# Kernel tuning notes

Hardware: AMD Instinct MI355X
Metric: run time of the kernel (lower is better)

The kernel has to match this reference:

```python
import jax, jax.numpy as jnp
import numpy as np

N_USER = 50000
N_ITEM = 50000
E = 500000
D_IN = 256
H = 4
D_HID = 64
D_OUT = 128
NEG_SLOPE = 0.2  # DGL GATConv default leaky_relu slope


def setup_inputs() -> dict:
    key = jax.random.key(0)
    ks = jax.random.split(key, 14)
    f = lambda k, s: jax.random.normal(k, s, dtype=jnp.float32)
    return {
        "h_src_user": f(ks[0], (N_USER, D_IN)),
        "h_src_item": f(ks[1], (N_ITEM, D_IN)),
        "h_dst_user": f(ks[2], (N_USER, D_IN)),
        "h_dst_item": f(ks[3], (N_ITEM, D_IN)),
        "u2i_src": jax.random.randint(ks[4], (E,), 0, N_USER),
        "u2i_dst": jax.random.randint(ks[5], (E,), 0, N_ITEM),
        "i2u_src": jax.random.randint(ks[6], (E,), 0, N_ITEM),
        "i2u_dst": jax.random.randint(ks[7], (E,), 0, N_USER),
        "fc_w": f(ks[8], (D_IN, H * D_HID)) * 0.05,
        "attn_l": f(ks[9], (H, D_HID)) * 0.05,
        "attn_r": f(ks[10], (H, D_HID)) * 0.05,
        "gat_bias": jnp.zeros((H * D_HID,), jnp.float32),
        "W_w": f(ks[11], (D_IN + D_HID, D_OUT)) * 0.05,
        "W_b": jnp.zeros((D_OUT,), jnp.float32),
    }


def _gat(feat_src, feat_dst, src, dst, n_dst, fc_w, attn_l, attn_r, gat_bias):
    # DGL GATConv (dropout is identity in eval mode)
    H_, D_ = attn_l.shape
    fs = (feat_src @ fc_w).reshape(-1, H_, D_)  # [Ns,H,D]
    fd = (feat_dst @ fc_w).reshape(-1, H_, D_)  # [Nd,H,D]
    el = jnp.sum(fs * attn_l, axis=-1)          # [Ns,H]
    er = jnp.sum(fd * attn_r, axis=-1)          # [Nd,H]
    e = jax.nn.leaky_relu(el[src] + er[dst], NEG_SLOPE)  # [E,H]
    # edge softmax per (dst node, head)
    m = jax.ops.segment_max(e, dst, num_segments=n_dst)
    m = jnp.where(jnp.isfinite(m), m, 0.0)      # guard zero-degree dst
    ex = jnp.exp(e - m[dst])
    den = jax.ops.segment_sum(ex, dst, num_segments=n_dst)
    alpha = ex / jnp.where(den == 0, 1.0, den)[dst]      # [E,H]
    out = jax.ops.segment_sum(alpha[:, :, None] * fs[src], dst, num_segments=n_dst)
    return out + gat_bias.reshape(1, H_, D_)    # [Nd,H,D]


def _head(agg, h_dst, W_w, W_b):
    # mean over heads, concat with dst feats, linear+relu, safe L2 normalize
    z = jax.nn.relu(jnp.concatenate([agg.mean(axis=1), h_dst], axis=1) @ W_w + W_b)
    n = jnp.linalg.norm(z, axis=1, keepdims=True)
    return z / jnp.where(n == 0, 1.0, n)


def reference(h_src_user, h_src_item, h_dst_user, h_dst_item,
              u2i_src, u2i_dst, i2u_src, i2u_dst,
              fc_w, attn_l, attn_r, gat_bias, W_w, W_b):
    agg_item = _gat(h_src_user, h_dst_item, u2i_src, u2i_dst, N_ITEM, fc_w, attn_l, attn_r, gat_bias)
    agg_user = _gat(h_src_item, h_dst_user, i2u_src, i2u_dst, N_USER, fc_w, attn_l, attn_r, gat_bias)
    z_user = _head(agg_user, h_dst_user, W_w, W_b)
    z_item = _head(agg_item, h_dst_item, W_w, W_b)
    return z_user, z_item
```

## Files before the change

### kernel.cpp

```cpp
#include <hip/hip_runtime.h>

#define NN 50000
#define N2 100000
#define EE 500000
#define E2 1000000

typedef unsigned short u16;
typedef unsigned int u32;

typedef __attribute__((ext_vector_type(8))) __bf16 bf16x8;
typedef __attribute__((ext_vector_type(4))) float f32x4;

__device__ __forceinline__ float4 ld4(const float* p) { return *(const float4*)p; }

__device__ __forceinline__ u16 f2bf(float f) {
  u32 u = __float_as_uint(f);
  u += 0x7FFFu + ((u >> 16) & 1u);
  return (u16)(u >> 16);
}

__device__ __forceinline__ u32 cvtpk(float lo, float hi) {
  u32 r;
  asm("v_cvt_pk_bf16_f32 %0, %1, %2" : "=v"(r) : "v"(lo), "v"(hi));
  return r;
}

__global__ void L384_const(const float* fc_w, const float* attn_l,
                           const float* attn_r, const float* Ww, float* w_r,
                           u16* wlB, u16* Bt, u16* Wt) {
  const int b = blockIdx.x;
  const int t = threadIdx.x;
  if (b < 256) {
    Bt[b * 256 + t] = f2bf(fc_w[(size_t)t * 256 + b]);
  } else if (b == 256) {
    for (int h = 0; h < 4; ++h) {
      float sl = 0.f, sr = 0.f;
      for (int d = 0; d < 64; ++d) {
        float f = fc_w[t * 256 + h * 64 + d];
        sl += f * attn_l[h * 64 + d];
        sr += f * attn_r[h * 64 + d];
      }
      w_r[t * 4 + h] = sr;
      wlB[h * 256 + t] = f2bf(sl);
    }
    for (int h = 4; h < 16; ++h) wlB[h * 256 + t] = 0;
  } else {
    int n = b - 257;
    for (int k = t; k < 320; k += 256)
      Wt[(size_t)n * 320 + k] = f2bf(Ww[(size_t)k * 128 + n]);
  }
}

__global__ void L384_prep(const float* Du, const float* Di, const float* w_r_,
                          u16* X, float* er) {
  const int r = blockIdx.x * 4 + (threadIdx.x >> 6);
  const int lane = threadIdx.x & 63;
  if (r >= N2) return;
  const float* src = (r < NN) ? Du + (size_t)r * 256 : Di + (size_t)(r - NN) * 256;
  float4 xv = ld4(src + lane * 4);
  uint2 pk = make_uint2(cvtpk(xv.x, xv.y), cvtpk(xv.z, xv.w));
  *(uint2*)(X + (size_t)r * 320 + 64 + lane * 4) = pk;
  const float* wr = w_r_ + lane * 16;
  float4 w0 = ld4(wr), w1 = ld4(wr + 4), w2 = ld4(wr + 8), w3 = ld4(wr + 12);
  float a0 = xv.x * w0.x + xv.y * w1.x + xv.z * w2.x + xv.w * w3.x;
  float a1 = xv.x * w0.y + xv.y * w1.y + xv.z * w2.y + xv.w * w3.y;
  float a2 = xv.x * w0.z + xv.y * w1.z + xv.z * w2.z + xv.w * w3.z;
  float a3 = xv.x * w0.w + xv.y * w1.w + xv.z * w2.w + xv.w * w3.w;
  for (int off = 32; off; off >>= 1) {
    a0 += __shfl_xor(a0, off);
    a1 += __shfl_xor(a1, off);
    a2 += __shfl_xor(a2, off);
    a3 += __shfl_xor(a3, off);
  }
  if (lane == 0) {
    float* op = er + (size_t)r * 4;
    op[0] = a0; op[1] = a1; op[2] = a2; op[3] = a3;
  }
}

__global__ __launch_bounds__(512) void L384_gemm(const float* Au, const float* Ai,
                                                 const u16* Bt, const u16* wlB,
                                                 u16* C, float* el) {
  __shared__ u16 bs[64][264];
  const int t = threadIdx.x;
  const int w = t >> 6;
  const int l = t & 63;
  const int lr = l & 15;
  const int kg = l >> 4;
  const int row0 = blockIdx.x * 128;

  const int row = row0 + w * 16 + lr;
  const int rr = (row < N2) ? row : (N2 - 1);
  const float* arow =
      ((rr < NN) ? Au + (size_t)rr * 256 : Ai + (size_t)(rr - NN) * 256) + kg * 8;
  uint4 a[8];
#pragma unroll
  for (int ks = 0; ks < 8; ++ks) {
    float4 f0 = ld4(arow + ks * 32);
    float4 f1 = ld4(arow + ks * 32 + 4);
    a[ks] = make_uint4(cvtpk(f0.x, f0.y), cvtpk(f0.z, f0.w), cvtpk(f1.x, f1.y),
                       cvtpk(f1.z, f1.w));
  }

  {
    f32x4 eacc = {0.f, 0.f, 0.f, 0.f};
    const u16* wl = wlB + lr * 256 + kg * 8;
#pragma unroll
    for (int ks = 0; ks < 8; ++ks) {
      union { bf16x8 v; uint4 q; } af, wf;
      af.q = a[ks];
      wf.q = *(const uint4*)(wl + ks * 32);
      eacc = __builtin_amdgcn_mfma_f32_16x16x32_bf16(af.v, wf.v, eacc, 0, 0, 0);
    }
    if (lr < 4) {
#pragma unroll
      for (int r = 0; r < 4; ++r) {
        int grow = row0 + w * 16 + kg * 4 + r;
        if (grow < N2) el[(size_t)grow * 4 + lr] = eacc[r];
      }
    }
  }

  for (int strip = 0; strip < 4; ++strip) {
    __syncthreads();
    {
      const int brow = t >> 3;
      const int bc = (t & 7) * 32;
      const uint4* s = (const uint4*)(Bt + (size_t)(strip * 64 + brow) * 256 + bc);
      uint4* d = (uint4*)&bs[brow][bc];
      d[0] = s[0]; d[1] = s[1]; d[2] = s[2]; d[3] = s[3];
    }
    __syncthreads();

    f32x4 acc[4];
#pragma unroll
    for (int ct = 0; ct < 4; ++ct) acc[ct] = (f32x4){0.f, 0.f, 0.f, 0.f};
#pragma unroll
    for (int ks = 0; ks < 8; ++ks) {
      union { bf16x8 v; uint4 q; } af;
      af.q = a[ks];
#pragma unroll
      for (int ct = 0; ct < 4; ++ct) {
        union { bf16x8 v; uint4 q; } b;
        b.q = *(const uint4*)&bs[ct * 16 + lr][ks * 32 + kg * 8];
        acc[ct] = __builtin_amdgcn_mfma_f32_16x16x32_bf16(af.v, b.v, acc[ct], 0, 0, 0);
      }
    }

#pragma unroll
    for (int p = 0; p < 2; ++p) {
      __syncthreads();
      if ((w >> 2) == p) {
        const int lrow = (w & 3) * 16 + kg * 4;
#pragma unroll
        for (int ct = 0; ct < 4; ++ct)
#pragma unroll
          for (int r = 0; r < 4; ++r)
            bs[lrow + r][ct * 16 + lr] = f2bf(acc[ct][r]);
      }
      __syncthreads();
      const int lrow2 = t >> 3;
      const int c0 = (t & 7) * 8;
      const int grow = row0 + p * 64 + lrow2;
      if (grow < N2)
        *(uint4*)(C + (size_t)grow * 256 + strip * 64 + c0) =
            *(const uint4*)&bs[lrow2][c0];
    }
  }
}

__global__ void L384_zero(int* p, int n) {
  int i = blockIdx.x * 256 + threadIdx.x;
  if (i < n) p[i] = 0;
}
__global__ void L384_hist(const int* i2u_dst, const int* u2i_dst, int* cnt) {
  int e = blockIdx.x * 256 + threadIdx.x;
  if (e < EE) {
    int d = i2u_dst[e];
    d = ((unsigned)d < NN) ? d : 0;
    atomicAdd(&cnt[d], 1);
  } else if (e < E2) {
    int d = u2i_dst[e - EE];
    d = ((unsigned)d < NN) ? d : 0;
    atomicAdd(&cnt[NN + d], 1);
  }
}
__global__ void L384_scan1(const int* cnt, int* part, int* bsum, int n) {
  __shared__ int sh[256];
  const int t = threadIdx.x;
  const int base = blockIdx.x * 1024 + t * 4;
  int v0 = (base + 0 < n) ? cnt[base + 0] : 0;
  int v1 = (base + 1 < n) ? cnt[base + 1] : 0;
  int v2 = (base + 2 < n) ? cnt[base + 2] : 0;
  int v3 = (base + 3 < n) ? cnt[base + 3] : 0;
  int s0 = v0, s1 = s0 + v1, s2 = s1 + v2, s3 = s2 + v3;
  sh[t] = s3;
  __syncthreads();
  for (int off = 1; off < 256; off <<= 1) {
    int x = (t >= off) ? sh[t - off] : 0;
    __syncthreads();
    sh[t] += x;
    __syncthreads();
  }
  int excl = (t > 0) ? sh[t - 1] : 0;
  if (base + 0 < n) part[base + 0] = excl;
  if (base + 1 < n) part[base + 1] = excl + s0;
  if (base + 2 < n) part[base + 2] = excl + s1;
  if (base + 3 < n) part[base + 3] = excl + s2;
  if (t == 255) bsum[blockIdx.x] = sh[255];
}
__global__ void L384_scan2(int* bsum, int nb, int* indptr, int n) {
  if (threadIdx.x == 0 && blockIdx.x == 0) {
    int acc = 0;
    for (int i = 0; i < nb; ++i) {
      int c = bsum[i];
      bsum[i] = acc;
      acc += c;
    }
    indptr[n] = acc;
  }
}
__global__ void L384_scan3(int* indptr, const int* bsum, int* cur, int n) {
  int i = blockIdx.x * 256 + threadIdx.x;
  if (i < n) {
    int v = indptr[i] + bsum[i >> 10];
    indptr[i] = v;
    cur[i] = v;
  }
}
__global__ void L384_fill(const int* i2u_src, const int* i2u_dst,
                          const int* u2i_src, const int* u2i_dst,
                          int* cur, int* csr) {
  int e = blockIdx.x * 256 + threadIdx.x;
  if (e < EE) {
    int d = i2u_dst[e];
    d = ((unsigned)d < NN) ? d : 0;
    int s = i2u_src[e];
    s = ((unsigned)s < NN) ? s : 0;
    int pos = atomicAdd(&cur[d], 1);
    if ((unsigned)pos < E2) csr[pos] = NN + s;
  } else if (e < E2) {
    int d = u2i_dst[e - EE];
    d = ((unsigned)d < NN) ? d : 0;
    int s = u2i_src[e - EE];
    s = ((unsigned)s < NN) ? s : 0;
    int pos = atomicAdd(&cur[NN + d], 1);
    if ((unsigned)pos < E2) csr[pos] = s;
  }
}
__global__ void L384_sort(const int* indptr, int* csr, int n) {
  __shared__ int buf[5120];
  const int t = threadIdx.x;
  const int node0 = blockIdx.x * 256;
  const int nEnd = (node0 + 256 < n) ? (node0 + 256) : n;
  if (node0 >= n) return;
  const int segL = indptr[node0];
  const int segR = indptr[nEnd];
  const int len = segR - segL;
  if (len <= 5120) {
    for (int i = t; i < len; i += 256) buf[i] = csr[segL + i];
    __syncthreads();
    const int node = node0 + t;
    if (node < n) {
      int p0 = indptr[node] - segL;
      int p1 = indptr[node + 1] - segL;
      for (int a = p0 + 1; a < p1; ++a) {
        int v = buf[a];
        int b = a - 1;
        while (b >= p0 && buf[b] > v) {
          buf[b + 1] = buf[b];
          --b;
        }
        buf[b + 1] = v;
      }
    }
    __syncthreads();
    for (int i = t; i < len; i += 256) csr[segL + i] = buf[i];
  } else {
    const int node = node0 + t;
    if (node < n) {
      int p0 = indptr[node], p1 = indptr[node + 1];
      for (int a = p0 + 1; a < p1; ++a) {
        int v = csr[a];
        int b = a - 1;
        while (b >= p0 && csr[b] > v) {
          csr[b + 1] = csr[b];
          --b;
        }
        csr[b + 1] = v;
      }
    }
  }
}

__global__ void L384_aggx(const int* indptr, const int* csr, const float* el,
                          const float* er, const u16* fs, const float* bias,
                          float* alphaG, u16* X) {
  __shared__ float aL[4][64][4];
  __shared__ int sL[4][64];
  const int slot = threadIdx.x >> 6;
  const int wid = blockIdx.x * 4 + slot;
  const int lane = threadIdx.x & 63;
  if (wid >= N2) return;
  const int p0 = indptr[wid];
  const int deg = indptr[wid + 1] - p0;
  const int h = lane >> 4;
  const int c = lane & 15;
  float4 er4 = ld4(er + (size_t)wid * 4);

  const bool small = (deg <= 64);
  if (small) {
    float4 ex = {0.f, 0.f, 0.f, 0.f};
    int s = 0;
    if (lane < deg) {
      s = csr[p0 + lane];
      s = ((unsigned)s < N2) ? s : 0;
      float4 ev = ld4(el + (size_t)s * 4);
      float e0 = ev.x + er4.x; e0 = (e0 >= 0.f) ? e0 : 0.2f * e0;
      float e1 = ev.y + er4.y; e1 = (e1 >= 0.f) ? e1 : 0.2f * e1;
      float e2 = ev.z + er4.z; e2 = (e2 >= 0.f) ? e2 : 0.2f * e2;
      float e3 = ev.w + er4.w; e3 = (e3 >= 0.f) ? e3 : 0.2f * e3;
      ex = make_float4(__expf(e0), __expf(e1), __expf(e2), __expf(e3));
    }
    float d0 = ex.x, d1 = ex.y, d2 = ex.z, d3 = ex.w;
    for (int off = 32; off; off >>= 1) {
      d0 += __shfl_xor(d0, off);
      d1 += __shfl_xor(d1, off);
      d2 += __shfl_xor(d2, off);
      d3 += __shfl_xor(d3, off);
    }
    if (lane < deg) {
      float4 o = make_float4(ex.x / d0, ex.y / d1, ex.z / d2, ex.w / d3);
      *(float4*)&aL[slot][lane][0] = o;
      sL[slot][lane] = s;
    }
  } else if (deg > 0) {
    float d0 = 0.f, d1 = 0.f, d2 = 0.f, d3 = 0.f;
    for (int i = lane; i < deg; i += 64) {
      int s = csr[p0 + i];
      s = ((unsigned)s < N2) ? s : 0;
      float4 ev = ld4(el + (size_t)s * 4);
      float e0 = ev.x + er4.x; e0 = (e0 >= 0.f) ? e0 : 0.2f * e0;
      float e1 = ev.y + er4.y; e1 = (e1 >= 0.f) ? e1 : 0.2f * e1;
      float e2 = ev.z + er4.z; e2 = (e2 >= 0.f) ? e2 : 0.2f * e2;
      float e3 = ev.w + er4.w; e3 = (e3 >= 0.f) ? e3 : 0.2f * e3;
      float4 ex = make_float4(__expf(e0), __expf(e1), __expf(e2), __expf(e3));
      *(float4*)(alphaG + (size_t)(p0 + i) * 4) = ex;
      d0 += ex.x; d1 += ex.y; d2 += ex.z; d3 += ex.w;
    }
    for (int off = 32; off; off >>= 1) {
      d0 += __shfl_xor(d0, off);
      d1 += __shfl_xor(d1, off);
      d2 += __shfl_xor(d2, off);
      d3 += __shfl_xor(d3, off);
    }
    float i0 = 1.f / d0, i1 = 1.f / d1, i2 = 1.f / d2, i3 = 1.f / d3;
    for (int i = lane; i < deg; i += 64) {
      float4 ex = *(const float4*)(alphaG + (size_t)(p0 + i) * 4);
      *(float4*)(alphaG + (size_t)(p0 + i) * 4) =
          make_float4(ex.x * i0, ex.y * i1, ex.z * i2, ex.w * i3);
    }
  }

  float ax = 0.f, ay = 0.f, az = 0.f, aw = 0.f;
  int i = 0;
  for (; i + 4 <= deg; i += 4) {
    int s0, s1, s2, s3;
    float a0, a1, a2, a3;
    if (small) {
      s0 = sL[slot][i + 0]; s1 = sL[slot][i + 1];
      s2 = sL[slot][i + 2]; s3 = sL[slot][i + 3];
      a0 = aL[slot][i + 0][h]; a1 = aL[slot][i + 1][h];
      a2 = aL[slot][i + 2][h]; a3 = aL[slot][i + 3][h];
    } else {
      s0 = csr[p0 + i + 0]; s0 = ((unsigned)s0 < N2) ? s0 : 0;
      s1 = csr[p0 + i + 1]; s1 = ((unsigned)s1 < N2) ? s1 : 0;
      s2 = csr[p0 + i + 2]; s2 = ((unsigned)s2 < N2) ? s2 : 0;
      s3 = csr[p0 + i + 3]; s3 = ((unsigned)s3 < N2) ? s3 : 0;
      a0 = alphaG[(size_t)(p0 + i + 0) * 4 + h];
      a1 = alphaG[(size_t)(p0 + i + 1) * 4 + h];
      a2 = alphaG[(size_t)(p0 + i + 2) * 4 + h];
      a3 = alphaG[(size_t)(p0 + i + 3) * 4 + h];
    }
    uint2 q0 = *(const uint2*)(fs + (size_t)s0 * 256 + lane * 4);
    uint2 q1 = *(const uint2*)(fs + (size_t)s1 * 256 + lane * 4);
    uint2 q2 = *(const uint2*)(fs + (size_t)s2 * 256 + lane * 4);
    uint2 q3 = *(const uint2*)(fs + (size_t)s3 * 256 + lane * 4);
    ax += a0 * __uint_as_float(q0.x << 16);
    ay += a0 * __uint_as_float(q0.x & 0xffff0000u);
    az += a0 * __uint_as_float(q0.y << 16);
    aw += a0 * __uint_as_float(q0.y & 0xffff0000u);
    ax += a1 * __uint_as_float(q1.x << 16);
    ay += a1 * __uint_as_float(q1.x & 0xffff0000u);
    az += a1 * __uint_as_float(q1.y << 16);
    aw += a1 * __uint_as_float(q1.y & 0xffff0000u);
    ax += a2 * __uint_as_float(q2.x << 16);
    ay += a2 * __uint_as_float(q2.x & 0xffff0000u);
    az += a2 * __uint_as_float(q2.y << 16);
    aw += a2 * __uint_as_float(q2.y & 0xffff0000u);
    ax += a3 * __uint_as_float(q3.x << 16);
    ay += a3 * __uint_as_float(q3.x & 0xffff0000u);
    az += a3 * __uint_as_float(q3.y << 16);
    aw += a3 * __uint_as_float(q3.y & 0xffff0000u);
  }
  for (; i < deg; ++i) {
    int s0;
    float a0;
    if (small) {
      s0 = sL[slot][i];
      a0 = aL[slot][i][h];
    } else {
      s0 = csr[p0 + i]; s0 = ((unsigned)s0 < N2) ? s0 : 0;
      a0 = alphaG[(size_t)(p0 + i) * 4 + h];
    }
    uint2 q0 = *(const uint2*)(fs + (size_t)s0 * 256 + lane * 4);
    ax += a0 * __uint_as_float(q0.x << 16);
    ay += a0 * __uint_as_float(q0.x & 0xffff0000u);
    az += a0 * __uint_as_float(q0.y << 16);
    aw += a0 * __uint_as_float(q0.y & 0xffff0000u);
  }
  const float* bp = bias + lane * 4;
  float ox = ax + bp[0];
  float oy = ay + bp[1];
  float oz = az + bp[2];
  float ow = aw + bp[3];
  for (int off = 16; off <= 32; off <<= 1) {
    ox += __shfl_xor(ox, off);
    oy += __shfl_xor(oy, off);
    oz += __shfl_xor(oz, off);
    ow += __shfl_xor(ow, off);
  }
  if (h == 0) {
    uint2 pk = make_uint2(cvtpk(ox * 0.25f, oy * 0.25f), cvtpk(oz * 0.25f, ow * 0.25f));
    *(uint2*)(X + (size_t)wid * 320 + 4 * c) = pk;
  }
}

__global__ void L384_headm(const u16* X, const u16* Wt, const float* Wb, float* out) {
  __shared__ float red[4][64];
  const int t = threadIdx.x;
  const int w = t >> 6;
  const int l = t & 63;
  const int row0 = blockIdx.x * 64;
  const int lr = l & 15;
  const int kg = l >> 4;
  f32x4 acc[4][2];
#pragma unroll
  for (int rg = 0; rg < 4; ++rg) {
    acc[rg][0] = (f32x4){0.f, 0.f, 0.f, 0.f};
    acc[rg][1] = (f32x4){0.f, 0.f, 0.f, 0.f};
  }
  const u16* arow[4];
#pragma unroll
  for (int rg = 0; rg < 4; ++rg) {
    int r = row0 + rg * 16 + lr;
    if (r >= N2) r = N2 - 1;
    arow[rg] = X + (size_t)r * 320 + kg * 8;
  }
  const u16* b0row = Wt + (size_t)(w * 32 + lr) * 320 + kg * 8;
  const u16* b1row = Wt + (size_t)(w * 32 + 16 + lr) * 320 + kg * 8;
#pragma unroll
  for (int k0 = 0; k0 < 320; k0 += 32) {
    union { bf16x8 v; uint4 q; } af[4], b0, b1;
#pragma unroll
    for (int rg = 0; rg < 4; ++rg) af[rg].q = *(const uint4*)(arow[rg] + k0);
    b0.q = *(const uint4*)(b0row + k0);
    b1.q = *(const uint4*)(b1row + k0);
#pragma unroll
    for (int rg = 0; rg < 4; ++rg) {
      acc[rg][0] = __builtin_amdgcn_mfma_f32_16x16x32_bf16(af[rg].v, b0.v,
                                                           acc[rg][0], 0, 0, 0);
      acc[rg][1] = __builtin_amdgcn_mfma_f32_16x16x32_bf16(af[rg].v, b1.v,
                                                           acc[rg][1], 0, 0, 0);
    }
  }
  const int col0 = w * 32 + lr;
  const int col1 = col0 + 16;
  float wb0 = Wb[col0], wb1 = Wb[col1];
  float z0[4][4], z1[4][4];
#pragma unroll
  for (int rg = 0; rg < 4; ++rg) {
    float pssq[4];
#pragma unroll
    for (int r = 0; r < 4; ++r) {
      z0[rg][r] = fmaxf(acc[rg][0][r] + wb0, 0.f);
      z1[rg][r] = fmaxf(acc[rg][1][r] + wb1, 0.f);
      pssq[r] = z0[rg][r] * z0[rg][r] + z1[rg][r] * z1[rg][r];
    }
#pragma unroll
    for (int off = 8; off; off >>= 1) {
#pragma unroll
      for (int r = 0; r < 4; ++r) pssq[r] += __shfl_xor(pssq[r], off);
    }
    if (lr == 0) {
#pragma unroll
      for (int r = 0; r < 4; ++r) red[w][rg * 16 + kg * 4 + r] = pssq[r];
    }
  }
  __syncthreads();
#pragma unroll
  for (int rg = 0; rg < 4; ++rg) {
#pragma unroll
    for (int r = 0; r < 4; ++r) {
      int lrow = rg * 16 + kg * 4 + r;
      int grow = row0 + lrow;
      if (grow < N2) {
        float ssq = red[0][lrow] + red[1][lrow] + red[2][lrow] + red[3][lrow];
        float inv = (ssq > 0.f) ? rsqrtf(ssq) : 0.f;
        float* op = out + (size_t)grow * 128;
        op[col0] = z0[rg][r] * inv;
        op[col1] = z1[rg][r] * inv;
      }
    }
  }
}

extern "C" void kernel_launch(void* const* d_in, const int* in_sizes, int n_in,
                              void* d_out, int out_size, void* d_ws, size_t ws_size,
                              hipStream_t stream) {
  (void)in_sizes; (void)n_in; (void)out_size; (void)ws_size;
  const float* h_src_user = (const float*)d_in[0];
  const float* h_src_item = (const float*)d_in[1];
  const float* h_dst_user = (const float*)d_in[2];
  const float* h_dst_item = (const float*)d_in[3];
  const int* u2i_src = (const int*)d_in[4];
  const int* u2i_dst = (const int*)d_in[5];
  const int* i2u_src = (const int*)d_in[6];
  const int* i2u_dst = (const int*)d_in[7];
  const float* fc_w = (const float*)d_in[8];
  const float* attn_l = (const float*)d_in[9];
  const float* attn_r = (const float*)d_in[10];
  const float* gat_bias = (const float*)d_in[11];
  const float* W_w = (const float*)d_in[12];
  const float* W_b = (const float*)d_in[13];
  float* out = (float*)d_out;

  float* el = (float*)d_ws;
  float* er = el + (size_t)N2 * 4;
  float* w_r = er + (size_t)N2 * 4;
  u16* wlB = (u16*)(w_r + 1024);
  float* alpha = (float*)(wlB + 16 * 256);
  u16* fs = (u16*)(alpha + (size_t)E2 * 4);
  u16* X = fs + (size_t)N2 * 256;
  u16* Bt = X + (size_t)N2 * 320;
  u16* Wt = Bt + 256 * 256;
  int* indptr = (int*)(Wt + 128 * 320);
  int* cur = indptr + (N2 + 4);
  int* csr = cur + N2;
  int* bsum = csr + E2;

  L384_const<<<385, 256, 0, stream>>>(fc_w, attn_l, attn_r, W_w, w_r, wlB, Bt, Wt);
  L384_prep<<<25000, 256, 0, stream>>>(h_dst_user, h_dst_item, w_r, X, er);

  L384_zero<<<391, 256, 0, stream>>>(cur, N2);
  L384_hist<<<3907, 256, 0, stream>>>(i2u_dst, u2i_dst, cur);
  L384_scan1<<<98, 256, 0, stream>>>(cur, indptr, bsum, N2);
  L384_scan2<<<1, 1, 0, stream>>>(bsum, 98, indptr, N2);
  L384_scan3<<<391, 256, 0, stream>>>(indptr, bsum, cur, N2);
  L384_fill<<<3907, 256, 0, stream>>>(i2u_src, i2u_dst, u2i_src, u2i_dst, cur, csr);
  L384_sort<<<391, 256, 0, stream>>>(indptr, csr, N2);

  L384_gemm<<<782, 512, 0, stream>>>(h_src_user, h_src_item, Bt, wlB, fs, el);
  L384_aggx<<<25000, 256, 0, stream>>>(indptr, csr, el, er, fs, gat_bias, alpha, X);
  L384_headm<<<1563, 256, 0, stream>>>(X, Wt, W_b, out);
}
```

Baseline: 386.6 us.

## Fuse CSR-build kernels into const, prep, and GEMM launches via extra blocks

Merges the zero, histogram, scan2/scan3 and fill kernels into existing launches by appending extra blocks: zeroing goes into the const kernel, the histogram into prep, the scan phases into a single scan23 kernel, and the CSR fill into the GEMM launch. This cuts the number of kernel launches and lets independent graph-building work overlap with the dense GEMM and prep work. The cost is that fill blocks now share the launch with GEMM blocks that use 512 threads and large shared memory, which may affect occupancy and scheduling. Each scan23 block also recomputes the 98-entry block prefix serially in one thread.

```diff
diff --git a/kernel.cpp b/kernel.cpp
--- a/kernel.cpp
+++ b/kernel.cpp
@@ -27,7 +27,7 @@
 
 __global__ void L384_const(const float* fc_w, const float* attn_l,
                            const float* attn_r, const float* Ww, float* w_r,
-                           u16* wlB, u16* Bt, u16* Wt) {
+                           u16* wlB, u16* Bt, u16* Wt, int* cur) {
   const int b = blockIdx.x;
   const int t = threadIdx.x;
   if (b < 256) {
@@ -44,16 +44,34 @@
       wlB[h * 256 + t] = f2bf(sl);
     }
     for (int h = 4; h < 16; ++h) wlB[h * 256 + t] = 0;
-  } else {
+  } else if (b < 385) {
     int n = b - 257;
     for (int k = t; k < 320; k += 256)
       Wt[(size_t)n * 320 + k] = f2bf(Ww[(size_t)k * 128 + n]);
+  } else {
+    int i = (b - 385) * 256 + t;
+    if (i < N2) cur[i] = 0;
   }
 }
 
 __global__ void L384_prep(const float* Du, const float* Di, const float* w_r_,
-                          u16* X, float* er) {
-  const int r = blockIdx.x * 4 + (threadIdx.x >> 6);
+                          u16* X, float* er, const int* i2u_dst,
+                          const int* u2i_dst, int* cnt) {
+  const int b = blockIdx.x;
+  if (b >= 25000) {
+    int e = (b - 25000) * 256 + threadIdx.x;
+    if (e < EE) {
+      int d = i2u_dst[e];
+      d = ((unsigned)d < NN) ? d : 0;
+      atomicAdd(&cnt[d], 1);
+    } else if (e < E2) {
+      int d = u2i_dst[e - EE];
+      d = ((unsigned)d < NN) ? d : 0;
+      atomicAdd(&cnt[NN + d], 1);
+    }
+    return;
+  }
+  const int r = b * 4 + (threadIdx.x >> 6);
   const int lane = threadIdx.x & 63;
   if (r >= N2) return;
   const float* src = (r < NN) ? Du + (size_t)r * 256 : Di + (size_t)(r - NN) * 256;
@@ -78,113 +96,6 @@
   }
 }
 
-__global__ __launch_bounds__(512) void L384_gemm(const float* Au, const float* Ai,
-                                                 const u16* Bt, const u16* wlB,
-                                                 u16* C, float* el) {
-  __shared__ u16 bs[64][264];
-  const int t = threadIdx.x;
-  const int w = t >> 6;
-  const int l = t & 63;
-  const int lr = l & 15;
-  const int kg = l >> 4;
-  const int row0 = blockIdx.x * 128;
-
-  const int row = row0 + w * 16 + lr;
-  const int rr = (row < N2) ? row : (N2 - 1);
-  const float* arow =
-      ((rr < NN) ? Au + (size_t)rr * 256 : Ai + (size_t)(rr - NN) * 256) + kg * 8;
-  uint4 a[8];
-#pragma unroll
-  for (int ks = 0; ks < 8; ++ks) {
-    float4 f0 = ld4(arow + ks * 32);
-    float4 f1 = ld4(arow + ks * 32 + 4);
-    a[ks] = make_uint4(cvtpk(f0.x, f0.y), cvtpk(f0.z, f0.w), cvtpk(f1.x, f1.y),
-                       cvtpk(f1.z, f1.w));
-  }
-
-  {
-    f32x4 eacc = {0.f, 0.f, 0.f, 0.f};
-    const u16* wl = wlB + lr * 256 + kg * 8;
-#pragma unroll
-    for (int ks = 0; ks < 8; ++ks) {
-      union { bf16x8 v; uint4 q; } af, wf;
-      af.q = a[ks];
-      wf.q = *(const uint4*)(wl + ks * 32);
-      eacc = __builtin_amdgcn_mfma_f32_16x16x32_bf16(af.v, wf.v, eacc, 0, 0, 0);
-    }
-    if (lr < 4) {
-#pragma unroll
-      for (int r = 0; r < 4; ++r) {
-        int grow = row0 + w * 16 + kg * 4 + r;
-        if (grow < N2) el[(size_t)grow * 4 + lr] = eacc[r];
-      }
-    }
-  }
-
-  for (int strip = 0; strip < 4; ++strip) {
-    __syncthreads();
-    {
-      const int brow = t >> 3;
-      const int bc = (t & 7) * 32;
-      const uint4* s = (const uint4*)(Bt + (size_t)(strip * 64 + brow) * 256 + bc);
-      uint4* d = (uint4*)&bs[brow][bc];
-      d[0] = s[0]; d[1] = s[1]; d[2] = s[2]; d[3] = s[3];
-    }
-    __syncthreads();
-
-    f32x4 acc[4];
-#pragma unroll
-    for (int ct = 0; ct < 4; ++ct) acc[ct] = (f32x4){0.f, 0.f, 0.f, 0.f};
-#pragma unroll
-    for (int ks = 0; ks < 8; ++ks) {
-      union { bf16x8 v; uint4 q; } af;
-      af.q = a[ks];
-#pragma unroll
-      for (int ct = 0; ct < 4; ++ct) {
-        union { bf16x8 v; uint4 q; } b;
-        b.q = *(const uint4*)&bs[ct * 16 + lr][ks * 32 + kg * 8];
-        acc[ct] = __builtin_amdgcn_mfma_f32_16x16x32_bf16(af.v, b.v, acc[ct], 0, 0, 0);
-      }
-    }
-
-#pragma unroll
-    for (int p = 0; p < 2; ++p) {
-      __syncthreads();
-      if ((w >> 2) == p) {
-        const int lrow = (w & 3) * 16 + kg * 4;
-#pragma unroll
-        for (int ct = 0; ct < 4; ++ct)
-#pragma unroll
-          for (int r = 0; r < 4; ++r)
-            bs[lrow + r][ct * 16 + lr] = f2bf(acc[ct][r]);
-      }
-      __syncthreads();
-      const int lrow2 = t >> 3;
-      const int c0 = (t & 7) * 8;
-      const int grow = row0 + p * 64 + lrow2;
-      if (grow < N2)
-        *(uint4*)(C + (size_t)grow * 256 + strip * 64 + c0) =
-            *(const uint4*)&bs[lrow2][c0];
-    }
-  }
-}
-
-__global__ void L384_zero(int* p, int n) {
-  int i = blockIdx.x * 256 + threadIdx.x;
-  if (i < n) p[i] = 0;
-}
-__global__ void L384_hist(const int* i2u_dst, const int* u2i_dst, int* cnt) {
-  int e = blockIdx.x * 256 + threadIdx.x;
-  if (e < EE) {
-    int d = i2u_dst[e];
-    d = ((unsigned)d < NN) ? d : 0;
-    atomicAdd(&cnt[d], 1);
-  } else if (e < E2) {
-    int d = u2i_dst[e - EE];
-    d = ((unsigned)d < NN) ? d : 0;
-    atomicAdd(&cnt[NN + d], 1);
-  }
-}
 __global__ void L384_scan1(const int* cnt, int* part, int* bsum, int n) {
   __shared__ int sh[256];
   const int t = threadIdx.x;
@@ -209,45 +120,140 @@
   if (base + 3 < n) part[base + 3] = excl + s2;
   if (t == 255) bsum[blockIdx.x] = sh[255];
 }
-__global__ void L384_scan2(int* bsum, int nb, int* indptr, int n) {
-  if (threadIdx.x == 0 && blockIdx.x == 0) {
+__global__ void L384_scan23(int* indptr, const int* bsum, int* cur, int nb, int n) {
+  __shared__ int pre[128];
+  const int t = threadIdx.x;
+  if (t == 0) {
     int acc = 0;
     for (int i = 0; i < nb; ++i) {
-      int c = bsum[i];
-      bsum[i] = acc;
-      acc += c;
-    }
-    indptr[n] = acc;
-  }
-}
-__global__ void L384_scan3(int* indptr, const int* bsum, int* cur, int n) {
-  int i = blockIdx.x * 256 + threadIdx.x;
+      pre[i] = acc;
+      acc += bsum[i];
+    }
+    pre[nb] = acc;
+  }
+  __syncthreads();
+  int i = blockIdx.x * 256 + t;
   if (i < n) {
-    int v = indptr[i] + bsum[i >> 10];
+    int v = indptr[i] + pre[i >> 10];
     indptr[i] = v;
     cur[i] = v;
   }
-}
-__global__ void L384_fill(const int* i2u_src, const int* i2u_dst,
-                          const int* u2i_src, const int* u2i_dst,
-                          int* cur, int* csr) {
-  int e = blockIdx.x * 256 + threadIdx.x;
-  if (e < EE) {
-    int d = i2u_dst[e];
-    d = ((unsigned)d < NN) ? d : 0;
-    int s = i2u_src[e];
-    s = ((unsigned)s < NN) ? s : 0;
-    int pos = atomicAdd(&cur[d], 1);
-    if ((unsigned)pos < E2) csr[pos] = NN + s;
-  } else if (e < E2) {
-    int d = u2i_dst[e - EE];
-    d = ((unsigned)d < NN) ? d : 0;
-    int s = u2i_src[e - EE];
-    s = ((unsigned)s < NN) ? s : 0;
-    int pos = atomicAdd(&cur[NN + d], 1);
-    if ((unsigned)pos < E2) csr[pos] = s;
-  }
-}
+  if (blockIdx.x == 0 && t == 0) indptr[n] = pre[nb];
+}
+
+__global__ __launch_bounds__(512) void L384_gemm(const float* Au, const float* Ai,
+                                                 const u16* Bt, const u16* wlB,
+                                                 u16* C, float* el,
+                                                 const int* i2u_src, const int* i2u_dst,
+                                                 const int* u2i_src, const int* u2i_dst,
+                                                 int* cur, int* csr) {
+  __shared__ u16 bs[64][264];
+  const int t = threadIdx.x;
+  if (blockIdx.x >= 782) {
+    int e = (blockIdx.x - 782) * 512 + t;
+    if (e < EE) {
+      int d = i2u_dst[e];
+      d = ((unsigned)d < NN) ? d : 0;
+      int s = i2u_src[e];
+      s = ((unsigned)s < NN) ? s : 0;
+      int pos = atomicAdd(&cur[d], 1);
+      if ((unsigned)pos < E2) csr[pos] = NN + s;
+    } else if (e < E2) {
+      int d = u2i_dst[e - EE];
+      d = ((unsigned)d < NN) ? d : 0;
+      int s = u2i_src[e - EE];
+      s = ((unsigned)s < NN) ? s : 0;
+      int pos = atomicAdd(&cur[NN + d], 1);
+      if ((unsigned)pos < E2) csr[pos] = s;
+    }
+    return;
+  }
+  const int w = t >> 6;
+  const int l = t & 63;
+  const int lr = l & 15;
+  const int kg = l >> 4;
+  const int row0 = blockIdx.x * 128;
+
+  const int row = row0 + w * 16 + lr;
+  const int rr = (row < N2) ? row : (N2 - 1);
+  const float* arow =
+      ((rr < NN) ? Au + (size_t)rr * 256 : Ai + (size_t)(rr - NN) * 256) + kg * 8;
+  uint4 a[8];
+#pragma unroll
+  for (int ks = 0; ks < 8; ++ks) {
+    float4 f0 = ld4(arow + ks * 32);
+    float4 f1 = ld4(arow + ks * 32 + 4);
+    a[ks] = make_uint4(cvtpk(f0.x, f0.y), cvtpk(f0.z, f0.w), cvtpk(f1.x, f1.y),
+                       cvtpk(f1.z, f1.w));
+  }
+
+  {
+    f32x4 eacc = {0.f, 0.f, 0.f, 0.f};
+    const u16* wl = wlB + lr * 256 + kg * 8;
+#pragma unroll
+    for (int ks = 0; ks < 8; ++ks) {
+      union { bf16x8 v; uint4 q; } af, wf;
+      af.q = a[ks];
+      wf.q = *(const uint4*)(wl + ks * 32);
+      eacc = __builtin_amdgcn_mfma_f32_16x16x32_bf16(af.v, wf.v, eacc, 0, 0, 0);
+    }
+    if (lr < 4) {
+#pragma unroll
+      for (int r = 0; r < 4; ++r) {
+        int grow = row0 + w * 16 + kg * 4 + r;
+        if (grow < N2) el[(size_t)grow * 4 + lr] = eacc[r];
+      }
+    }
+  }
+
+  for (int strip = 0; strip < 4; ++strip) {
+    __syncthreads();
+    {
+      const int brow = t >> 3;
+      const int bc = (t & 7) * 32;
+      const uint4* s = (const uint4*)(Bt + (size_t)(strip * 64 + brow) * 256 + bc);
+      uint4* d = (uint4*)&bs[brow][bc];
+      d[0] = s[0]; d[1] = s[1]; d[2] = s[2]; d[3] = s[3];
+    }
+    __syncthreads();
+
+    f32x4 acc[4];
+#pragma unroll
+    for (int ct = 0; ct < 4; ++ct) acc[ct] = (f32x4){0.f, 0.f, 0.f, 0.f};
+#pragma unroll
+    for (int ks = 0; ks < 8; ++ks) {
+      union { bf16x8 v; uint4 q; } af;
+      af.q = a[ks];
+#pragma unroll
+      for (int ct = 0; ct < 4; ++ct) {
+        union { bf16x8 v; uint4 q; } b;
+        b.q = *(const uint4*)&bs[ct * 16 + lr][ks * 32 + kg * 8];
+        acc[ct] = __builtin_amdgcn_mfma_f32_16x16x32_bf16(af.v, b.v, acc[ct], 0, 0, 0);
+      }
+    }
+
+#pragma unroll
+    for (int p = 0; p < 2; ++p) {
+      __syncthreads();
+      if ((w >> 2) == p) {
+        const int lrow = (w & 3) * 16 + kg * 4;
+#pragma unroll
+        for (int ct = 0; ct < 4; ++ct)
+#pragma unroll
+          for (int r = 0; r < 4; ++r)
+            bs[lrow + r][ct * 16 + lr] = f2bf(acc[ct][r]);
+      }
+      __syncthreads();
+      const int lrow2 = t >> 3;
+      const int c0 = (t & 7) * 8;
+      const int grow = row0 + p * 64 + lrow2;
+      if (grow < N2)
+        *(uint4*)(C + (size_t)grow * 256 + strip * 64 + c0) =
+            *(const uint4*)&bs[lrow2][c0];
+    }
+  }
+}
+
 __global__ void L384_sort(const int* indptr, int* csr, int n) {
   __shared__ int buf[5120];
   const int t = threadIdx.x;
@@ -549,18 +555,14 @@
   int* csr = cur + N2;
   int* bsum = csr + E2;
 
-  L384_const<<<385, 256, 0, stream>>>(fc_w, attn_l, attn_r, W_w, w_r, wlB, Bt, Wt);
-  L384_prep<<<25000, 256, 0, stream>>>(h_dst_user, h_dst_item, w_r, X, er);
-
-  L384_zero<<<391, 256, 0, stream>>>(cur, N2);
-  L384_hist<<<3907, 256, 0, stream>>>(i2u_dst, u2i_dst, cur);
+  L384_const<<<776, 256, 0, stream>>>(fc_w, attn_l, attn_r, W_w, w_r, wlB, Bt, Wt, cur);
+  L384_prep<<<28907, 256, 0, stream>>>(h_dst_user, h_dst_item, w_r, X, er,
+                                       i2u_dst, u2i_dst, cur);
   L384_scan1<<<98, 256, 0, stream>>>(cur, indptr, bsum, N2);
-  L384_scan2<<<1, 1, 0, stream>>>(bsum, 98, indptr, N2);
-  L384_scan3<<<391, 256, 0, stream>>>(indptr, bsum, cur, N2);
-  L384_fill<<<3907, 256, 0, stream>>>(i2u_src, i2u_dst, u2i_src, u2i_dst, cur, csr);
+  L384_scan23<<<391, 256, 0, stream>>>(indptr, bsum, cur, 98, N2);
+  L384_gemm<<<2736, 512, 0, stream>>>(h_src_user, h_src_item, Bt, wlB, fs, el,
+                                      i2u_src, i2u_dst, u2i_src, u2i_dst, cur, csr);
   L384_sort<<<391, 256, 0, stream>>>(indptr, csr, N2);
-
-  L384_gemm<<<782, 512, 0, stream>>>(h_src_user, h_src_item, Bt, wlB, fs, el);
   L384_aggx<<<25000, 256, 0, stream>>>(indptr, csr, el, er, fs, gat_bias, alpha, X);
   L384_headm<<<1563, 256, 0, stream>>>(X, Wt, W_b, out);
 }
```

Result: faster. 364.1 us (-5.8%).
